# Performance work log

Measured on AMD Instinct MI355X. Metric: run time of the kernel, lower is better.

## Reference

```python
import jax, jax.numpy as jnp
import numpy as np

N = 100000   # nodes
E = 1600000  # edges (before self-loops)
F = 128      # num_features
H = 128      # hidden_dim
EPS = 1e-5   # BatchNorm eps


def setup_inputs() -> dict:
    key = jax.random.key(0)
    ks = jax.random.split(key, 8)
    x = jax.random.normal(ks[0], (N, F), dtype=jnp.float32)
    edge_index = jax.random.randint(ks[1], (2, E), 0, N, dtype=jnp.int64)

    def lin(k, din, dout):
        s = 1.0 / np.sqrt(din)
        kw, kb = jax.random.split(k)
        W = jax.random.uniform(kw, (din, dout), jnp.float32, -s, s)
        b = jax.random.uniform(kb, (dout,), jnp.float32, -s, s)
        return W, b

    W1, b1 = lin(ks[2], F, H)
    W2, b2 = lin(ks[3], H, H)
    W3, b3 = lin(ks[4], H, H)
    Wc, bc = lin(ks[5], H, 2)

    def bn_params():
        return (jnp.ones((H,), jnp.float32), jnp.zeros((H,), jnp.float32),
                jnp.zeros((H,), jnp.float32), jnp.ones((H,), jnp.float32))

    g1, be1, rm1, rv1 = bn_params()
    g2, be2, rm2, rv2 = bn_params()
    g3, be3, rm3, rv3 = bn_params()

    return {"x": x, "edge_index": edge_index,
            "W1": W1, "b1": b1, "W2": W2, "b2": b2, "W3": W3, "b3": b3,
            "g1": g1, "be1": be1, "rm1": rm1, "rv1": rv1,
            "g2": g2, "be2": be2, "rm2": rm2, "rv2": rv2,
            "g3": g3, "be3": be3, "rm3": rm3, "rv3": rv3,
            "Wc": Wc, "bc": bc}


def _gcn_norm(edge_index, num_nodes):
    # add self-loops, compute symmetric normalization (PyG GCNConv default)
    loop = jnp.arange(num_nodes, dtype=edge_index.dtype)
    src = jnp.concatenate([edge_index[0], loop])
    dst = jnp.concatenate([edge_index[1], loop])
    deg = jax.ops.segment_sum(jnp.ones_like(dst, dtype=jnp.float32), dst,
                              num_segments=num_nodes)
    dinv = jnp.where(deg > 0, jax.lax.rsqrt(deg), 0.0)
    norm = dinv[src] * dinv[dst]  # [E+N]
    return src, dst, norm


def _gcn_conv(x, W, b, src, dst, norm, num_nodes):
    h = x @ W                              # [N, H] linear first
    msg = h[src] * norm[:, None]           # gather + scale  [E+N, H]
    out = jax.ops.segment_sum(msg, dst, num_segments=num_nodes)  # scatter-add
    return out + b


def _bn_eval(x, g, be, rm, rv):
    return (x - rm) * jax.lax.rsqrt(rv + EPS) * g + be


def reference(x, edge_index,
              W1, b1, W2, b2, W3, b3,
              g1, be1, rm1, rv1,
              g2, be2, rm2, rv2,
              g3, be3, rm3, rv3,
              Wc, bc):
    n = x.shape[0]
    src, dst, norm = _gcn_norm(edge_index, n)
    h = _gcn_conv(x, W1, b1, src, dst, norm, n)
    h = _bn_eval(jax.nn.relu(h), g1, be1, rm1, rv1)
    # dropout: identity in eval mode
    h = _gcn_conv(h, W2, b2, src, dst, norm, n)
    h = _bn_eval(jax.nn.relu(h), g2, be2, rm2, rv2)
    h = _gcn_conv(h, W3, b3, src, dst, norm, n)
    h = _bn_eval(jax.nn.relu(h), g3, be3, rm3, rv3)
    return h @ Wc + bc  # [N, 2]
```

## Files before the change

kernel.cpp:

```cpp
#include <hip/hip_runtime.h>
#include <hip/hip_fp16.h>

#define BN_EPS 1e-5f
#define CHUNK 2048
#define BBITS 7

typedef _Float16 half8 __attribute__((ext_vector_type(8)));
typedef _Float16 half2v __attribute__((ext_vector_type(2)));
typedef float f32x4 __attribute__((ext_vector_type(4)));

__device__ __forceinline__ float4 f4zero() { return make_float4(0.f, 0.f, 0.f, 0.f); }


__global__ __launch_bounds__(256) void k_bucket_hist(const int* __restrict__ dst,
                                                     int* __restrict__ tableT,
                                                     int nA, int nbuck, int e) {
    __shared__ int h[1024];
    int blk = blockIdx.x, tid = threadIdx.x;
    for (int k = tid; k < 1024; k += 256) h[k] = 0;
    __syncthreads();
    int base = blk * CHUNK;
    if (base + CHUNK <= e && (e & 3) == 0) {
        const int4* d4 = (const int4*)(dst + base);
#pragma unroll
        for (int t = 0; t < CHUNK / 1024; ++t) {
            int4 d = d4[t * 256 + tid];
            atomicAdd(&h[d.x >> BBITS], 1);
            atomicAdd(&h[d.y >> BBITS], 1);
            atomicAdd(&h[d.z >> BBITS], 1);
            atomicAdd(&h[d.w >> BBITS], 1);
        }
    } else {
        for (int i = base + tid; i < e && i < base + CHUNK; i += 256)
            atomicAdd(&h[dst[i] >> BBITS], 1);
    }
    __syncthreads();
    for (int k = tid; k < nbuck; k += 256)
        tableT[(size_t)k * nA + blk] = h[k];
}

__global__ __launch_bounds__(256) void k_bucket_scatter(const int* __restrict__ src,
                                                        const int* __restrict__ dst,
                                                        const int* __restrict__ tableT,
                                                        int2* __restrict__ bed,
                                                        int nA, int nbuck, int e) {
    __shared__ int cur[1024];
    int blk = blockIdx.x, tid = threadIdx.x;
    for (int k = tid; k < nbuck; k += 256)
        cur[k] = tableT[(size_t)k * nA + blk];
    __syncthreads();
    int base = blk * CHUNK;
    if (base + CHUNK <= e && (e & 3) == 0) {
        const int4* s4 = (const int4*)(src + base);
        const int4* d4 = (const int4*)(dst + base);
#pragma unroll
        for (int t = 0; t < CHUNK / 1024; ++t) {
            int4 s = s4[t * 256 + tid];
            int4 d = d4[t * 256 + tid];
            int p0 = atomicAdd(&cur[d.x >> BBITS], 1); bed[p0] = make_int2(s.x, d.x);
            int p1 = atomicAdd(&cur[d.y >> BBITS], 1); bed[p1] = make_int2(s.y, d.y);
            int p2 = atomicAdd(&cur[d.z >> BBITS], 1); bed[p2] = make_int2(s.z, d.z);
            int p3 = atomicAdd(&cur[d.w >> BBITS], 1); bed[p3] = make_int2(s.w, d.w);
        }
    } else {
        for (int i = base + tid; i < e && i < base + CHUNK; i += 256) {
            int d = dst[i];
            int p = atomicAdd(&cur[d >> BBITS], 1);
            bed[p] = make_int2(src[i], d);
        }
    }
}

__global__ __launch_bounds__(256) void k_bucket_rank(const int2* __restrict__ bed,
                                                     const int* __restrict__ tableT,
                                                     int* __restrict__ brank,
                                                     int* __restrict__ counts,
                                                     float* __restrict__ dinv,
                                                     int nA, int nbuck, int n, int e) {
    __shared__ int lcnt[128];
    int b = blockIdx.x, tid = threadIdx.x;
    if (tid < 128) lcnt[tid] = 0;
    __syncthreads();
    int start = tableT[(size_t)b * nA];
    int end = (b + 1 < nbuck) ? tableT[(size_t)(b + 1) * nA] : e;
    for (int i = start + tid; i < end; i += 256) {
        int2 q = bed[i];
        brank[i] = atomicAdd(&lcnt[q.y & ((1 << BBITS) - 1)], 1);
    }
    __syncthreads();
    if (tid < 128) {
        int node = (b << BBITS) + tid;
        if (node < n) {
            int c = lcnt[tid];
            counts[node] = c;
            dinv[node] = rsqrtf((float)(c + 1));
        }
    }
}

template <bool PAD8>
__global__ __launch_bounds__(1024) void k_scan_block(const int* __restrict__ counts,
                                                     int* __restrict__ offs,
                                                     int* __restrict__ partials, int len) {
    __shared__ int s[1024];
    int t = threadIdx.x;
    int gid = blockIdx.x * 1024 + t;
    int c = (gid < len) ? counts[gid] : 0;
    int v = PAD8 ? ((c + 7) & ~7) : c;
    int x = v;
    s[t] = x;
    __syncthreads();
    for (int d = 1; d < 1024; d <<= 1) {
        int y = (t >= d) ? s[t - d] : 0;
        __syncthreads();
        x += y;
        s[t] = x;
        __syncthreads();
    }
    if (gid < len) offs[gid] = x - v;
    if (t == 1023) partials[blockIdx.x] = x;
}

__global__ __launch_bounds__(1024) void k_scan_partials(int* __restrict__ partials, int nb) {
    __shared__ int s[1024];
    int t = threadIdx.x;
    int v = (t < nb) ? partials[t] : 0;
    int x = v;
    s[t] = x;
    __syncthreads();
    for (int d = 1; d < 1024; d <<= 1) {
        int y = (t >= d) ? s[t - d] : 0;
        __syncthreads();
        x += y;
        s[t] = x;
        __syncthreads();
    }
    if (t < nb) partials[t] = x - v;
    if (t == nb - 1) partials[nb] = x;
}

__global__ __launch_bounds__(256) void k_scan_add(int* __restrict__ offs,
                                                  const int* __restrict__ partials, int len) {
    int gid = blockIdx.x * 256 + threadIdx.x;
    if (gid < len) offs[gid] += partials[gid >> 10];
    if (gid == 0) offs[len] = partials[(len + 1023) >> 10];
}

__global__ __launch_bounds__(256) void k_fill(int4* __restrict__ er4, int val, int m4) {
    int i = blockIdx.x * 256 + threadIdx.x;
    if (i < m4) er4[i] = make_int4(val, val, val, val);
}

__global__ __launch_bounds__(256) void k_place2(const int2* __restrict__ bed,
                                                const int* __restrict__ brank,
                                                const int* __restrict__ offs,
                                                int* __restrict__ er, int e) {
    int i = (blockIdx.x * 256 + threadIdx.x) * 2;
    if (i + 1 < e) {
        int4 q = *(const int4*)(bed + i);
        int2 r = *(const int2*)(brank + i);
        er[offs[q.y] + r.x] = q.x;
        er[offs[q.w] + r.y] = q.z;
    } else if (i < e) {
        int2 q = bed[i];
        er[offs[q.y] + brank[i]] = q.x;
    }
}


__global__ __launch_bounds__(256) void k_packW(const float* __restrict__ W,
                                               _Float16* __restrict__ out) {
    int t = blockIdx.x * 256 + threadIdx.x;
    if (t >= 2048) return;
    int kc = t >> 9;
    int rem = t & 511;
    int ct = rem >> 6;
    int lane = rem & 63;
    int q = lane >> 4;
    int col = ct * 16 + (lane & 15);
    half8 h;
#pragma unroll
    for (int j = 0; j < 8; ++j)
        h[j] = (_Float16)W[(kc * 32 + q * 8 + j) * 128 + col];
    *(half8*)(out + (size_t)t * 8) = h;
}


template <bool AF32>
__global__ __launch_bounds__(256) void k_gemm_mfma(const void* __restrict__ Av,
                                                   const _Float16* __restrict__ pW,
                                                   const float* __restrict__ dinv,
                                                   uint4* __restrict__ C, int n) {
    __shared__ char smem[32768];
    uint4* sW = (uint4*)smem;
    int tid = threadIdx.x;

    {
        const uint4* gW = (const uint4*)pW;
#pragma unroll
        for (int i = 0; i < 8; ++i) sW[tid + 256 * i] = gW[tid + 256 * i];
    }
    __syncthreads();

    int wave = tid >> 6, lane = tid & 63;
    int quad = lane >> 4, l16 = lane & 15;
    int row0 = blockIdx.x * 64 + wave * 16;
    int arow = row0 + l16;
    int arowc = (arow < n) ? arow : (n - 1);

    half8 af[4];
    if (AF32) {
        const float* A = (const float*)Av + (size_t)arowc * 128 + quad * 8;
#pragma unroll
        for (int kc = 0; kc < 4; ++kc) {
            float4 lo = *(const float4*)(A + kc * 32);
            float4 hi = *(const float4*)(A + kc * 32 + 4);
            half8 h;
            h[0] = (_Float16)lo.x; h[1] = (_Float16)lo.y;
            h[2] = (_Float16)lo.z; h[3] = (_Float16)lo.w;
            h[4] = (_Float16)hi.x; h[5] = (_Float16)hi.y;
            h[6] = (_Float16)hi.z; h[7] = (_Float16)hi.w;
            af[kc] = h;
        }
    } else {
        const _Float16* A = (const _Float16*)Av + (size_t)arowc * 128 + quad * 8;
#pragma unroll
        for (int kc = 0; kc < 4; ++kc)
            af[kc] = *(const half8*)(A + kc * 32);
    }

    f32x4 acc[8];
#pragma unroll
    for (int ct = 0; ct < 8; ++ct) acc[ct] = (f32x4){0.f, 0.f, 0.f, 0.f};

#pragma unroll
    for (int kc = 0; kc < 4; ++kc) {
#pragma unroll
        for (int ct = 0; ct < 8; ++ct) {
            half8 bf = *(half8*)&sW[(kc * 8 + ct) * 64 + lane];
            acc[ct] = __builtin_amdgcn_mfma_f32_16x16x32_f16(af[kc], bf, acc[ct], 0, 0, 0);
        }
    }

    __syncthreads();

    _Float16* eb = (_Float16*)smem + wave * 16 * 136;
    float dv[4];
#pragma unroll
    for (int r = 0; r < 4; ++r) {
        int rr = row0 + quad * 4 + r;
        dv[r] = dinv[(rr < n) ? rr : (n - 1)];
    }
#pragma unroll
    for (int ct = 0; ct < 8; ++ct)
#pragma unroll
        for (int r = 0; r < 4; ++r)
            eb[(quad * 4 + r) * 136 + ct * 16 + l16] = (_Float16)(acc[ct][r] * dv[r]);

#pragma unroll
    for (int i = 0; i < 4; ++i) {
        int linear = i * 64 + lane;
        int r = linear >> 4, c = linear & 15;
        uint4 v = *(uint4*)((char*)eb + r * 272 + c * 16);
        int row = row0 + r;
        if (row < n) C[(size_t)row * 16 + c] = v;
    }
}


__device__ __forceinline__ void accum8(float* acc, uint4 q) {
    const half2v b0 = {(_Float16)1.0f, (_Float16)0.0f};
    const half2v b1 = {(_Float16)0.0f, (_Float16)1.0f};
    unsigned int u[4] = {q.x, q.y, q.z, q.w};
#pragma unroll
    for (int k = 0; k < 4; ++k) {
        half2v h = *(half2v*)&u[k];
        acc[2 * k + 0] = __builtin_amdgcn_fdot2(h, b0, acc[2 * k + 0], false);
        acc[2 * k + 1] = __builtin_amdgcn_fdot2(h, b1, acc[2 * k + 1], false);
    }
}

template <bool FUSE_CLS>
__global__ __launch_bounds__(256) void k_aggregate(const uint4* __restrict__ Ah4,
                                                   const int* __restrict__ offs,
                                                   const int* __restrict__ er,
                                                   const float* __restrict__ dinv,
                                                   const float* __restrict__ bias,
                                                   const float* __restrict__ g,
                                                   const float* __restrict__ be,
                                                   const float* __restrict__ rm,
                                                   const float* __restrict__ rv,
                                                   uint4* __restrict__ Hout,
                                                   const float* __restrict__ Wc,
                                                   const float* __restrict__ bc,
                                                   float* __restrict__ out, int n) {
    int lane32 = threadIdx.x & 31;
    int node = blockIdx.x * 8 + (threadIdx.x >> 5);
    if (node >= n) return;
    int sub = lane32 & 15;
    bool hi = lane32 >= 16;

    float acc[8];
#pragma unroll
    for (int j = 0; j < 8; ++j) acc[j] = 0.f;

    {
        uint4 qs = Ah4[(size_t)node * 16 + sub];
        if (!hi) accum8(acc, qs);
    }

    int e0 = offs[node], e1 = offs[node + 1];
    for (int e = e0; e < e1; e += 8) {
        int4 ra = *(const int4*)(er + e);
        int4 rb = *(const int4*)(er + e + 4);
        int r0 = hi ? ra.y : ra.x;
        int r1 = hi ? ra.w : ra.z;
        int r2 = hi ? rb.y : rb.x;
        int r3 = hi ? rb.w : rb.z;
        uint4 q0 = Ah4[(size_t)r0 * 16 + sub];
        uint4 q1 = Ah4[(size_t)r1 * 16 + sub];
        uint4 q2 = Ah4[(size_t)r2 * 16 + sub];
        uint4 q3 = Ah4[(size_t)r3 * 16 + sub];
        accum8(acc, q0); accum8(acc, q1); accum8(acc, q2); accum8(acc, q3);
    }

#pragma unroll
    for (int j = 0; j < 8; ++j) acc[j] += __shfl_xor(acc[j], 16, 32);

    float di = dinv[node];
    const float4* b4 = (const float4*)bias;
    const float4* g4 = (const float4*)g;
    const float4* be4 = (const float4*)be;
    const float4* rm4 = (const float4*)rm;
    const float4* rv4 = (const float4*)rv;

    float o[8];
#pragma unroll
    for (int h = 0; h < 2; ++h) {
        float4 bb = b4[sub * 2 + h], gg = g4[sub * 2 + h], ee = be4[sub * 2 + h];
        float4 mm = rm4[sub * 2 + h], vv = rv4[sub * 2 + h];
        float v;
        v = fmaxf(acc[4 * h + 0] * di + bb.x, 0.f); o[4 * h + 0] = (v - mm.x) * rsqrtf(vv.x + BN_EPS) * gg.x + ee.x;
        v = fmaxf(acc[4 * h + 1] * di + bb.y, 0.f); o[4 * h + 1] = (v - mm.y) * rsqrtf(vv.y + BN_EPS) * gg.y + ee.y;
        v = fmaxf(acc[4 * h + 2] * di + bb.z, 0.f); o[4 * h + 2] = (v - mm.z) * rsqrtf(vv.z + BN_EPS) * gg.z + ee.z;
        v = fmaxf(acc[4 * h + 3] * di + bb.w, 0.f); o[4 * h + 3] = (v - mm.w) * rsqrtf(vv.w + BN_EPS) * gg.w + ee.w;
    }

    if (!FUSE_CLS) {
        if (!hi) {
            __half2 p0 = __floats2half2_rn(o[0], o[1]);
            __half2 p1 = __floats2half2_rn(o[2], o[3]);
            __half2 p2 = __floats2half2_rn(o[4], o[5]);
            __half2 p3 = __floats2half2_rn(o[6], o[7]);
            uint4 u;
            u.x = *(unsigned int*)&p0; u.y = *(unsigned int*)&p1;
            u.z = *(unsigned int*)&p2; u.w = *(unsigned int*)&p3;
            Hout[(size_t)node * 16 + sub] = u;
        }
    } else {
        const float4* Wv = (const float4*)Wc;
        float p0 = 0.f, p1 = 0.f;
#pragma unroll
        for (int k = 0; k < 4; ++k) {
            float4 w = Wv[sub * 4 + k];
            p0 += o[2 * k] * w.x + o[2 * k + 1] * w.z;
            p1 += o[2 * k] * w.y + o[2 * k + 1] * w.w;
        }
#pragma unroll
        for (int d = 8; d >= 1; d >>= 1) {
            p0 += __shfl_down(p0, d, 16);
            p1 += __shfl_down(p1, d, 16);
        }
        if (lane32 == 0) {
            out[node * 2 + 0] = p0 + bc[0];
            out[node * 2 + 1] = p1 + bc[1];
        }
    }
}


extern "C" void kernel_launch(void* const* d_in, const int* in_sizes, int n_in,
                              void* d_out, int out_size, void* d_ws, size_t ws_size,
                              hipStream_t stream) {
    const float* x   = (const float*)d_in[0];
    const int*   ei  = (const int*)d_in[1];
    const float* W1  = (const float*)d_in[2];
    const float* b1  = (const float*)d_in[3];
    const float* W2  = (const float*)d_in[4];
    const float* b2  = (const float*)d_in[5];
    const float* W3  = (const float*)d_in[6];
    const float* b3  = (const float*)d_in[7];
    const float* g1  = (const float*)d_in[8];
    const float* be1 = (const float*)d_in[9];
    const float* rm1 = (const float*)d_in[10];
    const float* rv1 = (const float*)d_in[11];
    const float* g2  = (const float*)d_in[12];
    const float* be2 = (const float*)d_in[13];
    const float* rm2 = (const float*)d_in[14];
    const float* rv2 = (const float*)d_in[15];
    const float* g3  = (const float*)d_in[16];
    const float* be3 = (const float*)d_in[17];
    const float* rm3 = (const float*)d_in[18];
    const float* rv3 = (const float*)d_in[19];
    const float* Wc  = (const float*)d_in[20];
    const float* bc  = (const float*)d_in[21];
    float* out = (float*)d_out;

    int n = in_sizes[0] / 128;
    int e = in_sizes[1] / 2;
    const int* src = ei;
    const int* dst = ei + e;

    char* ws = (char*)d_ws;
    size_t off = 0;
    auto alloc = [&](size_t bytes) -> char* {
        char* p = ws + off;
        off += (bytes + 255) & ~(size_t)255;
        return p;
    };
    int erCap = e + 8 * n;
    uint2*     bufA   = (uint2*)alloc((size_t)(n + 1) * 128 * 2);
    char*      bufH   = (char*) alloc((size_t)n * 128 * 4);
    float*     dinv   = (float*)alloc((size_t)n * 4);
    int*       counts = (int*)  alloc((size_t)n * 4);
    int*       offs   = (int*)  alloc((size_t)(n + 1) * 4);
    int*       parts  = (int*)  alloc(8192);
    int*       er     = (int*)  alloc((size_t)erCap * 4);
    _Float16*  pW     = (_Float16*)alloc(3 * 16384 * 2);
    (void)ws_size; (void)n_in; (void)out_size;

    int nA    = (e + CHUNK - 1) / CHUNK;
    int nbuck = (n + (1 << BBITS) - 1) >> BBITS;
    int tlen  = nbuck * nA;
    {
        char* p = bufH + (size_t)n * 128 * 2;
        size_t po = 0;
        auto palloc = [&](size_t bytes) -> char* {
            char* q = p + po;
            po += (bytes + 255) & ~(size_t)255;
            return q;
        };
        int2* bed    = (int2*)palloc((size_t)e * 8);
        int*  brank  = (int*) palloc((size_t)e * 4);
        int*  tableT = (int*) palloc((size_t)(tlen + 1) * 4);

        hipMemsetAsync(bufA + (size_t)n * 32, 0, 256, stream);

        int gN  = (n + 255) / 256;
        int nb  = (n + 1023) / 1024;
        int nbT = (tlen + 1023) / 1024;
        int m4  = erCap / 4;

        k_packW<<<8, 256, 0, stream>>>(W1, pW);
        k_packW<<<8, 256, 0, stream>>>(W2, pW + 16384);
        k_packW<<<8, 256, 0, stream>>>(W3, pW + 32768);
        k_bucket_hist<<<nA, 256, 0, stream>>>(dst, tableT, nA, nbuck, e);
        k_scan_block<false><<<nbT, 1024, 0, stream>>>(tableT, tableT, parts, tlen);
        k_scan_partials<<<1, 1024, 0, stream>>>(parts, nbT);
        k_scan_add<<<(tlen + 255) / 256, 256, 0, stream>>>(tableT, parts, tlen);
        k_bucket_scatter<<<nA, 256, 0, stream>>>(src, dst, tableT, bed, nA, nbuck, e);
        k_bucket_rank<<<nbuck, 256, 0, stream>>>(bed, tableT, brank, counts, dinv, nA, nbuck, n, e);
        k_scan_block<true><<<nb, 1024, 0, stream>>>(counts, offs, parts, n);
        k_scan_partials<<<1, 1024, 0, stream>>>(parts, nb);
        k_scan_add<<<gN, 256, 0, stream>>>(offs, parts, n);
        k_fill<<<(m4 + 255) / 256, 256, 0, stream>>>((int4*)er, n, m4);
        k_place2<<<((e + 1) / 2 + 255) / 256, 256, 0, stream>>>(bed, brank, offs, er, e);
    }

    int gGemm = (n + 63) / 64;
    int gAgg  = (n + 7) / 8;

    k_gemm_mfma<true><<<gGemm, 256, 0, stream>>>(x, pW, dinv, (uint4*)bufA, n);
    k_aggregate<false><<<gAgg, 256, 0, stream>>>((const uint4*)bufA, offs, er, dinv,
                                                 b1, g1, be1, rm1, rv1, (uint4*)bufH,
                                                 nullptr, nullptr, nullptr, n);

    k_gemm_mfma<false><<<gGemm, 256, 0, stream>>>(bufH, pW + 16384, dinv, (uint4*)bufA, n);
    k_aggregate<false><<<gAgg, 256, 0, stream>>>((const uint4*)bufA, offs, er, dinv,
                                                 b2, g2, be2, rm2, rv2, (uint4*)bufH,
                                                 nullptr, nullptr, nullptr, n);

    k_gemm_mfma<false><<<gGemm, 256, 0, stream>>>(bufH, pW + 32768, dinv, (uint4*)bufA, n);
    k_aggregate<true><<<gAgg, 256, 0, stream>>>((const uint4*)bufA, offs, er, dinv,
                                                b3, g3, be3, rm3, rv3, nullptr,
                                                Wc, bc, out, n);
}
```

Baseline: 433.8 us.

## Split feature dimension into 8 column chunks for cache-friendly gather aggregation

Stores the fp16 hidden activations in a chunked layout (8 chunks of 16 features, each [n+1] rows of 32 bytes). Aggregation runs over a 2D grid, one chunk per blockIdx.y, so each pass gathers from a 3.2 MB slice that can stay in cache. The GEMM reads and writes this layout, and the fused classifier now writes per-chunk partials that a new reduce kernel sums. The cost is eight passes over the CSR edge list, narrower 4-byte gathers per lane, and an extra kernel plus partials buffer.

```diff
diff --git a/kernel.cpp b/kernel.cpp
--- a/kernel.cpp
+++ b/kernel.cpp
@@ -4,9 +4,9 @@
 #define BN_EPS 1e-5f
 #define CHUNK 2048
 #define BBITS 7
+#define NCH 8
 
 typedef _Float16 half8 __attribute__((ext_vector_type(8)));
-typedef _Float16 half2v __attribute__((ext_vector_type(2)));
 typedef float f32x4 __attribute__((ext_vector_type(4)));
 
 __device__ __forceinline__ float4 f4zero() { return make_float4(0.f, 0.f, 0.f, 0.f); }
@@ -167,6 +167,14 @@
     }
 }
 
+__global__ void k_zero_pad(unsigned int* __restrict__ A, int n) {
+    int tid = threadIdx.x;
+    if (tid < 64) {
+        int c = tid >> 3, sub = tid & 7;
+        A[((size_t)c * (n + 1) + n) * 8 + sub] = 0u;
+    }
+}
+
 
 __global__ __launch_bounds__(256) void k_packW(const float* __restrict__ W,
                                                _Float16* __restrict__ out) {
@@ -190,7 +198,7 @@
 __global__ __launch_bounds__(256) void k_gemm_mfma(const void* __restrict__ Av,
                                                    const _Float16* __restrict__ pW,
                                                    const float* __restrict__ dinv,
-                                                   uint4* __restrict__ C, int n) {
+                                                   uint2* __restrict__ C, int n) {
     __shared__ char smem[32768];
     uint4* sW = (uint4*)smem;
     int tid = threadIdx.x;
@@ -223,10 +231,13 @@
             af[kc] = h;
         }
     } else {
-        const _Float16* A = (const _Float16*)Av + (size_t)arowc * 128 + quad * 8;
-#pragma unroll
-        for (int kc = 0; kc < 4; ++kc)
-            af[kc] = *(const half8*)(A + kc * 32);
+        const _Float16* A = (const _Float16*)Av;
+        int c0 = quad >> 1, qh = quad & 1;
+#pragma unroll
+        for (int kc = 0; kc < 4; ++kc) {
+            size_t idx = ((size_t)(2 * kc + c0) * (n + 1) + arowc) * 16 + qh * 8;
+            af[kc] = *(const half8*)(A + idx);
+        }
     }
 
     f32x4 acc[8];
@@ -258,30 +269,20 @@
             eb[(quad * 4 + r) * 136 + ct * 16 + l16] = (_Float16)(acc[ct][r] * dv[r]);
 
 #pragma unroll
-    for (int i = 0; i < 4; ++i) {
-        int linear = i * 64 + lane;
-        int r = linear >> 4, c = linear & 15;
-        uint4 v = *(uint4*)((char*)eb + r * 272 + c * 16);
+    for (int i = 0; i < 8; ++i) {
+        int u = i * 64 + lane;
+        int r = u >> 5;
+        int b = u & 31;
+        int c = b >> 2, h = b & 3;
+        uint2 v = *(uint2*)((char*)eb + r * 272 + b * 8);
         int row = row0 + r;
-        if (row < n) C[(size_t)row * 16 + c] = v;
-    }
-}
-
-
-__device__ __forceinline__ void accum8(float* acc, uint4 q) {
-    const half2v b0 = {(_Float16)1.0f, (_Float16)0.0f};
-    const half2v b1 = {(_Float16)0.0f, (_Float16)1.0f};
-    unsigned int u[4] = {q.x, q.y, q.z, q.w};
-#pragma unroll
-    for (int k = 0; k < 4; ++k) {
-        half2v h = *(half2v*)&u[k];
-        acc[2 * k + 0] = __builtin_amdgcn_fdot2(h, b0, acc[2 * k + 0], false);
-        acc[2 * k + 1] = __builtin_amdgcn_fdot2(h, b1, acc[2 * k + 1], false);
-    }
-}
+        if (row < n) C[((size_t)c * (n + 1) + row) * 4 + h] = v;
+    }
+}
+
 
 template <bool FUSE_CLS>
-__global__ __launch_bounds__(256) void k_aggregate(const uint4* __restrict__ Ah4,
+__global__ __launch_bounds__(256) void k_aggregate(const unsigned int* __restrict__ Ah,
                                                    const int* __restrict__ offs,
                                                    const int* __restrict__ er,
                                                    const float* __restrict__ dinv,
@@ -290,92 +291,90 @@
                                                    const float* __restrict__ be,
                                                    const float* __restrict__ rm,
                                                    const float* __restrict__ rv,
-                                                   uint4* __restrict__ Hout,
+                                                   unsigned int* __restrict__ Hout,
                                                    const float* __restrict__ Wc,
-                                                   const float* __restrict__ bc,
-                                                   float* __restrict__ out, int n) {
-    int lane32 = threadIdx.x & 31;
-    int node = blockIdx.x * 8 + (threadIdx.x >> 5);
+                                                   float2* __restrict__ partials,
+                                                   int n) {
+    int c = blockIdx.y;
+    int sub = threadIdx.x & 7;
+    int node = blockIdx.x * 32 + (threadIdx.x >> 3);
     if (node >= n) return;
-    int sub = lane32 & 15;
-    bool hi = lane32 >= 16;
-
-    float acc[8];
-#pragma unroll
-    for (int j = 0; j < 8; ++j) acc[j] = 0.f;
-
+    size_t cbase = (size_t)c * (n + 1);
+
+    float a0, a1;
     {
-        uint4 qs = Ah4[(size_t)node * 16 + sub];
-        if (!hi) accum8(acc, qs);
+        unsigned q = Ah[(cbase + node) * 8 + sub];
+        float2 f = __half22float2(*(__half2*)&q);
+        a0 = f.x; a1 = f.y;
     }
 
     int e0 = offs[node], e1 = offs[node + 1];
     for (int e = e0; e < e1; e += 8) {
         int4 ra = *(const int4*)(er + e);
         int4 rb = *(const int4*)(er + e + 4);
-        int r0 = hi ? ra.y : ra.x;
-        int r1 = hi ? ra.w : ra.z;
-        int r2 = hi ? rb.y : rb.x;
-        int r3 = hi ? rb.w : rb.z;
-        uint4 q0 = Ah4[(size_t)r0 * 16 + sub];
-        uint4 q1 = Ah4[(size_t)r1 * 16 + sub];
-        uint4 q2 = Ah4[(size_t)r2 * 16 + sub];
-        uint4 q3 = Ah4[(size_t)r3 * 16 + sub];
-        accum8(acc, q0); accum8(acc, q1); accum8(acc, q2); accum8(acc, q3);
-    }
-
-#pragma unroll
-    for (int j = 0; j < 8; ++j) acc[j] += __shfl_xor(acc[j], 16, 32);
+        unsigned q0 = Ah[(cbase + ra.x) * 8 + sub];
+        unsigned q1 = Ah[(cbase + ra.y) * 8 + sub];
+        unsigned q2 = Ah[(cbase + ra.z) * 8 + sub];
+        unsigned q3 = Ah[(cbase + ra.w) * 8 + sub];
+        unsigned q4 = Ah[(cbase + rb.x) * 8 + sub];
+        unsigned q5 = Ah[(cbase + rb.y) * 8 + sub];
+        unsigned q6 = Ah[(cbase + rb.z) * 8 + sub];
+        unsigned q7 = Ah[(cbase + rb.w) * 8 + sub];
+        float2 f0 = __half22float2(*(__half2*)&q0);
+        float2 f1 = __half22float2(*(__half2*)&q1);
+        float2 f2 = __half22float2(*(__half2*)&q2);
+        float2 f3 = __half22float2(*(__half2*)&q3);
+        float2 f4 = __half22float2(*(__half2*)&q4);
+        float2 f5 = __half22float2(*(__half2*)&q5);
+        float2 f6 = __half22float2(*(__half2*)&q6);
+        float2 f7 = __half22float2(*(__half2*)&q7);
+        a0 += f0.x + f1.x + f2.x + f3.x + f4.x + f5.x + f6.x + f7.x;
+        a1 += f0.y + f1.y + f2.y + f3.y + f4.y + f5.y + f6.y + f7.y;
+    }
 
     float di = dinv[node];
-    const float4* b4 = (const float4*)bias;
-    const float4* g4 = (const float4*)g;
-    const float4* be4 = (const float4*)be;
-    const float4* rm4 = (const float4*)rm;
-    const float4* rv4 = (const float4*)rv;
-
-    float o[8];
-#pragma unroll
-    for (int h = 0; h < 2; ++h) {
-        float4 bb = b4[sub * 2 + h], gg = g4[sub * 2 + h], ee = be4[sub * 2 + h];
-        float4 mm = rm4[sub * 2 + h], vv = rv4[sub * 2 + h];
-        float v;
-        v = fmaxf(acc[4 * h + 0] * di + bb.x, 0.f); o[4 * h + 0] = (v - mm.x) * rsqrtf(vv.x + BN_EPS) * gg.x + ee.x;
-        v = fmaxf(acc[4 * h + 1] * di + bb.y, 0.f); o[4 * h + 1] = (v - mm.y) * rsqrtf(vv.y + BN_EPS) * gg.y + ee.y;
-        v = fmaxf(acc[4 * h + 2] * di + bb.z, 0.f); o[4 * h + 2] = (v - mm.z) * rsqrtf(vv.z + BN_EPS) * gg.z + ee.z;
-        v = fmaxf(acc[4 * h + 3] * di + bb.w, 0.f); o[4 * h + 3] = (v - mm.w) * rsqrtf(vv.w + BN_EPS) * gg.w + ee.w;
-    }
+    a0 *= di; a1 *= di;
+
+    int fi = c * 8 + sub;
+    float2 bb = ((const float2*)bias)[fi];
+    float2 gg = ((const float2*)g)[fi];
+    float2 ee = ((const float2*)be)[fi];
+    float2 mm = ((const float2*)rm)[fi];
+    float2 vv = ((const float2*)rv)[fi];
+
+    float v0 = fmaxf(a0 + bb.x, 0.f);
+    float v1 = fmaxf(a1 + bb.y, 0.f);
+    float o0 = (v0 - mm.x) * rsqrtf(vv.x + BN_EPS) * gg.x + ee.x;
+    float o1 = (v1 - mm.y) * rsqrtf(vv.y + BN_EPS) * gg.y + ee.y;
 
     if (!FUSE_CLS) {
-        if (!hi) {
-            __half2 p0 = __floats2half2_rn(o[0], o[1]);
-            __half2 p1 = __floats2half2_rn(o[2], o[3]);
-            __half2 p2 = __floats2half2_rn(o[4], o[5]);
-            __half2 p3 = __floats2half2_rn(o[6], o[7]);
-            uint4 u;
-            u.x = *(unsigned int*)&p0; u.y = *(unsigned int*)&p1;
-            u.z = *(unsigned int*)&p2; u.w = *(unsigned int*)&p3;
-            Hout[(size_t)node * 16 + sub] = u;
-        }
+        __half2 p = __floats2half2_rn(o0, o1);
+        Hout[(cbase + node) * 8 + sub] = *(unsigned int*)&p;
     } else {
-        const float4* Wv = (const float4*)Wc;
-        float p0 = 0.f, p1 = 0.f;
-#pragma unroll
-        for (int k = 0; k < 4; ++k) {
-            float4 w = Wv[sub * 4 + k];
-            p0 += o[2 * k] * w.x + o[2 * k + 1] * w.z;
-            p1 += o[2 * k] * w.y + o[2 * k + 1] * w.w;
-        }
-#pragma unroll
-        for (int d = 8; d >= 1; d >>= 1) {
-            p0 += __shfl_down(p0, d, 16);
-            p1 += __shfl_down(p1, d, 16);
-        }
-        if (lane32 == 0) {
-            out[node * 2 + 0] = p0 + bc[0];
-            out[node * 2 + 1] = p1 + bc[1];
-        }
-    }
+        float4 w = ((const float4*)Wc)[fi];
+        float p0 = o0 * w.x + o1 * w.z;
+        float p1 = o0 * w.y + o1 * w.w;
+#pragma unroll
+        for (int d = 4; d >= 1; d >>= 1) {
+            p0 += __shfl_down(p0, d, 8);
+            p1 += __shfl_down(p1, d, 8);
+        }
+        if (sub == 0) partials[(size_t)c * n + node] = make_float2(p0, p1);
+    }
+}
+
+__global__ __launch_bounds__(256) void k_reduce_out(const float2* __restrict__ partials,
+                                                    const float* __restrict__ bc,
+                                                    float2* __restrict__ out2, int n) {
+    int i = blockIdx.x * 256 + threadIdx.x;
+    if (i >= n) return;
+    float sx = 0.f, sy = 0.f;
+#pragma unroll
+    for (int c = 0; c < NCH; ++c) {
+        float2 p = partials[(size_t)c * n + i];
+        sx += p.x; sy += p.y;
+    }
+    out2[i] = make_float2(sx + bc[0], sy + bc[1]);
 }
 
 
@@ -419,8 +418,9 @@
         return p;
     };
     int erCap = e + 8 * n;
-    uint2*     bufA   = (uint2*)alloc((size_t)(n + 1) * 128 * 2);
-    char*      bufH   = (char*) alloc((size_t)n * 128 * 4);
+    char*      bufA   = (char*) alloc((size_t)(n + 1) * 128 * 2);
+    char*      bufH   = (char*) alloc((size_t)(n + 1) * 128 * 2 + 64);
+    char*      scr    = (char*) alloc((size_t)20 * 1024 * 1024);
     float*     dinv   = (float*)alloc((size_t)n * 4);
     int*       counts = (int*)  alloc((size_t)n * 4);
     int*       offs   = (int*)  alloc((size_t)(n + 1) * 4);
@@ -433,7 +433,7 @@
     int nbuck = (n + (1 << BBITS) - 1) >> BBITS;
     int tlen  = nbuck * nA;
     {
-        char* p = bufH + (size_t)n * 128 * 2;
+        char* p = scr;
         size_t po = 0;
         auto palloc = [&](size_t bytes) -> char* {
             char* q = p + po;
@@ -441,47 +441,59 @@
             return q;
         };
         int2* bed    = (int2*)palloc((size_t)e * 8);
-        int*  brank  = (int*) palloc((size_t)e * 4);
-        int*  tableT = (int*) palloc((size_t)(tlen + 1) * 4);
-
-        hipMemsetAsync(bufA + (size_t)n * 32, 0, 256, stream);
-
-        int gN  = (n + 255) / 256;
-        int nb  = (n + 1023) / 1024;
-        int nbT = (tlen + 1023) / 1024;
-        int m4  = erCap / 4;
-
-        k_packW<<<8, 256, 0, stream>>>(W1, pW);
-        k_packW<<<8, 256, 0, stream>>>(W2, pW + 16384);
-        k_packW<<<8, 256, 0, stream>>>(W3, pW + 32768);
-        k_bucket_hist<<<nA, 256, 0, stream>>>(dst, tableT, nA, nbuck, e);
-        k_scan_block<false><<<nbT, 1024, 0, stream>>>(tableT, tableT, parts, tlen);
-        k_scan_partials<<<1, 1024, 0, stream>>>(parts, nbT);
-        k_scan_add<<<(tlen + 255) / 256, 256, 0, stream>>>(tableT, parts, tlen);
-        k_bucket_scatter<<<nA, 256, 0, stream>>>(src, dst, tableT, bed, nA, nbuck, e);
-        k_bucket_rank<<<nbuck, 256, 0, stream>>>(bed, tableT, brank, counts, dinv, nA, nbuck, n, e);
-        k_scan_block<true><<<nb, 1024, 0, stream>>>(counts, offs, parts, n);
-        k_scan_partials<<<1, 1024, 0, stream>>>(parts, nb);
-        k_scan_add<<<gN, 256, 0, stream>>>(offs, parts, n);
-        k_fill<<<(m4 + 255) / 256, 256, 0, stream>>>((int4*)er, n, m4);
-        k_place2<<<((e + 1) / 2 + 255) / 256, 256, 0, stream>>>(bed, brank, offs, er, e);
+        int*  brank  = (int*) p;
+        {
+            char* p2 = bufH;
+            size_t po2 = 0;
+            auto palloc2 = [&](size_t bytes) -> char* {
+                char* q = p2 + po2;
+                po2 += (bytes + 255) & ~(size_t)255;
+                return q;
+            };
+            brank = (int*)palloc2((size_t)e * 4);
+            int* tableT = (int*)palloc2((size_t)(tlen + 1) * 4);
+
+            k_zero_pad<<<1, 64, 0, stream>>>((unsigned int*)bufA, n);
+
+            int gN  = (n + 255) / 256;
+            int nb  = (n + 1023) / 1024;
+            int nbT = (tlen + 1023) / 1024;
+            int m4  = erCap / 4;
+
+            k_packW<<<8, 256, 0, stream>>>(W1, pW);
+            k_packW<<<8, 256, 0, stream>>>(W2, pW + 16384);
+            k_packW<<<8, 256, 0, stream>>>(W3, pW + 32768);
+            k_bucket_hist<<<nA, 256, 0, stream>>>(dst, tableT, nA, nbuck, e);
+            k_scan_block<false><<<nbT, 1024, 0, stream>>>(tableT, tableT, parts, tlen);
+            k_scan_partials<<<1, 1024, 0, stream>>>(parts, nbT);
+            k_scan_add<<<(tlen + 255) / 256, 256, 0, stream>>>(tableT, parts, tlen);
+            k_bucket_scatter<<<nA, 256, 0, stream>>>(src, dst, tableT, bed, nA, nbuck, e);
+            k_bucket_rank<<<nbuck, 256, 0, stream>>>(bed, tableT, brank, counts, dinv, nA, nbuck, n, e);
+            k_scan_block<true><<<nb, 1024, 0, stream>>>(counts, offs, parts, n);
+            k_scan_partials<<<1, 1024, 0, stream>>>(parts, nb);
+            k_scan_add<<<gN, 256, 0, stream>>>(offs, parts, n);
+            k_fill<<<(m4 + 255) / 256, 256, 0, stream>>>((int4*)er, n, m4);
+            k_place2<<<((e + 1) / 2 + 255) / 256, 256, 0, stream>>>(bed, brank, offs, er, e);
+        }
     }
 
     int gGemm = (n + 63) / 64;
-    int gAgg  = (n + 7) / 8;
-
-    k_gemm_mfma<true><<<gGemm, 256, 0, stream>>>(x, pW, dinv, (uint4*)bufA, n);
-    k_aggregate<false><<<gAgg, 256, 0, stream>>>((const uint4*)bufA, offs, er, dinv,
-                                                 b1, g1, be1, rm1, rv1, (uint4*)bufH,
-                                                 nullptr, nullptr, nullptr, n);
-
-    k_gemm_mfma<false><<<gGemm, 256, 0, stream>>>(bufH, pW + 16384, dinv, (uint4*)bufA, n);
-    k_aggregate<false><<<gAgg, 256, 0, stream>>>((const uint4*)bufA, offs, er, dinv,
-                                                 b2, g2, be2, rm2, rv2, (uint4*)bufH,
-                                                 nullptr, nullptr, nullptr, n);
-
-    k_gemm_mfma<false><<<gGemm, 256, 0, stream>>>(bufH, pW + 32768, dinv, (uint4*)bufA, n);
-    k_aggregate<true><<<gAgg, 256, 0, stream>>>((const uint4*)bufA, offs, er, dinv,
-                                                b3, g3, be3, rm3, rv3, nullptr,
-                                                Wc, bc, out, n);
-}
+    dim3 gAgg((n + 31) / 32, NCH);
+
+    k_gemm_mfma<true><<<gGemm, 256, 0, stream>>>(x, pW, dinv, (uint2*)bufA, n);
+    k_aggregate<false><<<gAgg, 256, 0, stream>>>((const unsigned int*)bufA, offs, er, dinv,
+                                                 b1, g1, be1, rm1, rv1,
+                                                 (unsigned int*)bufH, nullptr, nullptr, n);
+
+    k_gemm_mfma<false><<<gGemm, 256, 0, stream>>>(bufH, pW + 16384, dinv, (uint2*)bufA, n);
+    k_aggregate<false><<<gAgg, 256, 0, stream>>>((const unsigned int*)bufA, offs, er, dinv,
+                                                 b2, g2, be2, rm2, rv2,
+                                                 (unsigned int*)bufH, nullptr, nullptr, n);
+
+    k_gemm_mfma<false><<<gGemm, 256, 0, stream>>>(bufH, pW + 32768, dinv, (uint2*)bufA, n);
+    float2* partials = (float2*)bufH;
+    k_aggregate<true><<<gAgg, 256, 0, stream>>>((const unsigned int*)bufA, offs, er, dinv,
+                                                b3, g3, be3, rm3, rv3,
+                                                nullptr, Wc, partials, n);
+    k_reduce_out<<<(n + 255) / 256, 256, 0, stream>>>(partials, bc, (float2*)out, n);
+}
```

After: 515.0 us. +18.7%, slower.
